# Optimization experiments

Measured on AMD Instinct MI355X. Metric: run time of the kernel, lower is better.

The kernel has to match this reference:

```python
import jax, jax.numpy as jnp
import numpy as np

K = 20
EPS = 1e-5
NEG_SLOPE = 0.2


def knn(x, k):
    # x: [B, C, N] -> idx [B, N, k] of nearest neighbors (negative sq-dist topk)
    inner = -2.0 * jnp.einsum('bcn,bcm->bnm', x, x)
    xx = jnp.sum(x * x, axis=1)  # [B, N]
    d = -xx[:, :, None] - inner - xx[:, None, :]
    return jax.lax.top_k(d, k)[1]


def get_graph_feature(x, k):
    # x: [B, C, N] -> [B, 2C, N, k]
    idx = knn(x, k)
    xt = jnp.transpose(x, (0, 2, 1))            # [B, N, C]
    feat = jax.vmap(lambda a, i: a[i])(xt, idx)  # [B, N, k, C]
    center = xt[:, :, None, :]
    out = jnp.concatenate([feat - center, jnp.broadcast_to(center, feat.shape)], axis=-1)
    return jnp.transpose(out, (0, 3, 1, 2))


def conv_bn_lrelu(x, w, g, b):
    # 1x1 conv + BatchNorm2d (batch stats, training mode) + LeakyReLU(0.2)
    y = jnp.einsum('oc,bcnk->bonk', w, x)
    mu = jnp.mean(y, axis=(0, 2, 3), keepdims=True)
    var = jnp.mean((y - mu) ** 2, axis=(0, 2, 3), keepdims=True)
    y = (y - mu) * jax.lax.rsqrt(var + EPS)
    y = y * g[None, :, None, None] + b[None, :, None, None]
    return jnp.where(y >= 0, y, NEG_SLOPE * y)


def lrelu(y):
    return jnp.where(y >= 0, y, NEG_SLOPE * y)


def setup_inputs() -> dict:
    key = jax.random.key(0)
    ks = jax.random.split(key, 24)
    B, N = 8, 4096
    d = {}
    d['x'] = jax.random.normal(ks[0], (B, 3, N), dtype=jnp.float32)
    def wconv(k_, o, c):
        return jax.random.normal(k_, (o, c), dtype=jnp.float32) * (1.0 / np.sqrt(c))
    d['w1'] = wconv(ks[1], 32, 6)
    d['g1'] = 1.0 + 0.1 * jax.random.normal(ks[2], (32,), dtype=jnp.float32)
    d['b1'] = 0.1 * jax.random.normal(ks[3], (32,), dtype=jnp.float32)
    d['w2'] = wconv(ks[4], 64, 70)
    d['g2'] = 1.0 + 0.1 * jax.random.normal(ks[5], (64,), dtype=jnp.float32)
    d['b2'] = 0.1 * jax.random.normal(ks[6], (64,), dtype=jnp.float32)
    d['wd1'] = wconv(ks[7], 64, 64)
    d['gd1'] = 1.0 + 0.1 * jax.random.normal(ks[8], (64,), dtype=jnp.float32)
    d['bd1'] = 0.1 * jax.random.normal(ks[9], (64,), dtype=jnp.float32)
    d['wd2'] = wconv(ks[10], 64, 128)
    d['gd2'] = 1.0 + 0.1 * jax.random.normal(ks[11], (64,), dtype=jnp.float32)
    d['bd2'] = 0.1 * jax.random.normal(ks[12], (64,), dtype=jnp.float32)
    d['W2d'] = jax.random.normal(ks[13], (128, 128), dtype=jnp.float32) * (1.0 / np.sqrt(128))
    d['b2d'] = 0.1 * jax.random.normal(ks[14], (128,), dtype=jnp.float32)
    d['W3d'] = jax.random.normal(ks[15], (64, 128), dtype=jnp.float32) * (1.0 / np.sqrt(128))
    d['b3d'] = 0.1 * jax.random.normal(ks[16], (64,), dtype=jnp.float32)
    d['W4d'] = jax.random.normal(ks[17], (11, 64), dtype=jnp.float32) * (1.0 / np.sqrt(64))
    d['b4d'] = 0.1 * jax.random.normal(ks[18], (11,), dtype=jnp.float32)
    return d


def reference(x, w1, g1, b1, w2, g2, b2, wd1, gd1, bd1, wd2, gd2, bd2,
              W2d, b2d, W3d, b3d, W4d, b4d):
    x1_gf = get_graph_feature(x, K)                    # [B, 6, N, k]
    x1_max = jnp.max(conv_bn_lrelu(x1_gf, w1, g1, b1), axis=-1)  # [B, 32, N]
    x2_gf = jnp.concatenate([x1_gf, get_graph_feature(x1_max, K)], axis=1)  # [B, 70, N, k]
    x2_max = jnp.max(conv_bn_lrelu(x2_gf, w2, g2, b2), axis=-1)  # [B, 64, N]
    xd1 = jnp.max(conv_bn_lrelu(get_graph_feature(x1_max, K), wd1, gd1, bd1), axis=-1)  # [B, 64, N]
    xd2 = jnp.max(conv_bn_lrelu(get_graph_feature(x2_max, K), wd2, gd2, bd2), axis=-1)  # [B, 64, N]
    h = jnp.concatenate([xd1, xd2], axis=1)            # [B, 128, N]
    h = h.reshape(1, -1, 128)                          # faithful row-major view
    h = jnp.mean(h, axis=1)                            # [1, 128]
    h = lrelu(h @ W2d.T + b2d)
    h = lrelu(h @ W3d.T + b3d)
    return lrelu(h @ W4d.T + b4d)                      # [1, 11]
```

## Files before the change

### kernel.cpp

```cpp
#include <hip/hip_runtime.h>

#define BB 8
#define NN 4096
#define KK 20
constexpr float EPSV = 1e-5f;
constexpr float SLOPE = 0.2f;

typedef __bf16 bfrag __attribute__((ext_vector_type(8)));
typedef float floatx4 __attribute__((ext_vector_type(4)));
typedef unsigned short us4 __attribute__((ext_vector_type(4)));
typedef unsigned short us8 __attribute__((ext_vector_type(8)));

__device__ __forceinline__ float lrelu(float v) { return v >= 0.f ? v : SLOPE * v; }

__device__ __forceinline__ unsigned short bf16rn(float f) {
    unsigned int u = __float_as_uint(f);
    return (unsigned short)((u + 0x7FFFu + ((u >> 16) & 1u)) >> 16);
}
__device__ __forceinline__ float bf16up(unsigned short h) {
    return __uint_as_float(((unsigned int)h) << 16);
}

__device__ __forceinline__ void gl_lds16(const unsigned short* g, unsigned short* l) {
    __builtin_amdgcn_global_load_lds((const __attribute__((address_space(1))) void*)g,
                                     (__attribute__((address_space(3))) void*)l, 16, 0, 0);
}

__global__ void zero_kernel(float* p, int n) {
    int i = blockIdx.x * 256 + threadIdx.x;
    if (i < n) p[i] = 0.f;
}

template<int C>
__global__ void pack_kernel(const float* __restrict__ src, unsigned short* __restrict__ pk) {
    constexpr int SK = 2 * C + 8;
    const int id = blockIdx.x;
    const int b = id & 7;
    const int m0 = (id >> 3) * 64;
    const int tid = threadIdx.x;
    for (int i = tid; i < 64 * (C / 4); i += 256) {
        int m = i & 63;
        int c4 = (i >> 6) * 4;
        us4 hv, lv;
        #pragma unroll
        for (int j = 0; j < 4; j++) {
            float v = src[(b * C + c4 + j) * NN + m0 + m];
            unsigned short h = bf16rn(v);
            hv[j] = h;
            lv[j] = bf16rn(v - bf16up(h));
        }
        *(us4*)(&pk[(size_t)(b * NN + m0 + m) * SK + c4]) = hv;
        *(us4*)(&pk[(size_t)(b * NN + m0 + m) * SK + C + c4]) = lv;
    }
    if (tid < 64) {
        float s = 0.f;
        for (int c = 0; c < C; c++) {
            float v = src[(b * C + c) * NN + m0 + tid];
            s += v * v;
        }
        unsigned int ub = __float_as_uint(0.5f * s);
        us8 z;
        #pragma unroll
        for (int j = 0; j < 8; j++) z[j] = 0;
        z[0] = (unsigned short)(ub & 0xFFFFu);
        z[1] = (unsigned short)(ub >> 16);
        *(us8*)(&pk[(size_t)(b * NN + m0 + tid) * SK + 2 * C]) = z;
    }
}

__global__ void pack3_kernel(const float* __restrict__ src, unsigned short* __restrict__ pk) {
    const int id = blockIdx.x;
    const int b = id & 7;
    const int m = (id >> 3) * 256 + threadIdx.x;
    us8 w0, w1;
    #pragma unroll
    for (int j = 0; j < 8; j++) { w0[j] = 0; w1[j] = 0; }
    unsigned short row[12];
    float s = 0.f;
    #pragma unroll
    for (int c = 0; c < 3; c++) {
        float v = src[(b * 3 + c) * NN + m];
        s += v * v;
        unsigned short h = bf16rn(v);
        unsigned short l = bf16rn(v - bf16up(h));
        row[c] = h; row[3 + c] = l; row[6 + c] = l; row[9 + c] = h;
    }
    #pragma unroll
    for (int j = 0; j < 8; j++) w0[j] = row[j];
    #pragma unroll
    for (int j = 0; j < 4; j++) w1[j] = row[8 + j];
    unsigned short* dst = pk + (size_t)(b * NN + m) * 40;
    us8 z;
    #pragma unroll
    for (int j = 0; j < 8; j++) z[j] = 0;
    unsigned int ub = __float_as_uint(0.5f * s);
    us8 zh = z;
    zh[0] = (unsigned short)(ub & 0xFFFFu);
    zh[1] = (unsigned short)(ub >> 16);
    *(us8*)(dst) = w0;
    *(us8*)(dst + 8) = w1;
    *(us8*)(dst + 16) = z;
    *(us8*)(dst + 24) = z;
    *(us8*)(dst + 32) = zh;
}

template<int C>
__global__ __launch_bounds__(256) void knn_kernel(const float* __restrict__ src,
                                                  const unsigned short* __restrict__ pk,
                                                  int* __restrict__ idx) {
    constexpr int SK = (C == 3) ? 40 : (2 * C + 8);
    constexpr int HNOFF = (C == 3) ? 32 : 2 * C;
    constexpr int UNITS = 8 * SK;
    constexpr int PF = (UNITS + 255) / 256;
    constexpr int KKN = (C == 3) ? 1 : (C / 32);
    __shared__ __attribute__((aligned(16))) unsigned short cpack[2 * 64 * SK];
    __shared__ float pv[64 * 65];
    __shared__ unsigned short pidx[64 * 66];
    __shared__ float tau[64];
    __shared__ int cnt[64];
    __shared__ unsigned short qls[(C == 3) ? 64 * 40 : 2];

    const int bid = blockIdx.x;
    const int b = bid & 7;
    const int q0 = (bid >> 3) * 64;
    const int tid = threadIdx.x;
    const int lane = tid & 63;
    const int wv = tid >> 6;
    const int wr = (wv >> 1) * 32;
    const int wc = (wv & 1) * 32;
    const int fl = lane & 15;
    const int fq = lane >> 4;

    float tv[20]; int ti[20];
    #pragma unroll
    for (int k = 0; k < 20; k++) { tv[k] = -3.4e38f; ti[k] = 0; }

    bfrag qah[KKN][2], qal[KKN][2];
    if (C == 3) {
        for (int i = tid; i < 64 * 20; i += 256) {
            int r = i / 20, k = 12 + i % 20;
            qls[r * 40 + k] = 0;
        }
        if (tid < 64) {
            #pragma unroll
            for (int c = 0; c < 3; c++) {
                float v = src[(b * 3 + c) * NN + q0 + tid];
                unsigned short h = bf16rn(v);
                unsigned short l = bf16rn(v - bf16up(h));
                qls[tid * 40 + c] = h;  qls[tid * 40 + 3 + c] = l;
                qls[tid * 40 + 6 + c] = h;  qls[tid * 40 + 9 + c] = l;
            }
        }
    } else {
        #pragma unroll
        for (int r2 = 0; r2 < 2; r2++) {
            const unsigned short* qr = pk + (size_t)(b * NN + q0 + wr + r2 * 16 + fl) * SK + fq * 8;
            #pragma unroll
            for (int kk = 0; kk < KKN; kk++) {
                qah[kk][r2] = *(const bfrag*)(qr + kk * 32);
                qal[kk][r2] = *(const bfrag*)(qr + C + kk * 32);
            }
        }
    }

    {
        const unsigned short* p0 = pk + (size_t)(b * NN) * SK;
        #pragma unroll
        for (int r = 0; r < PF; r++) {
            int u0 = r * 256 + wv * 64;
            if (u0 < UNITS)
                gl_lds16(p0 + (size_t)(u0 + lane) * 8, cpack + (size_t)u0 * 8);
        }
    }
    if (tid < 64) { tau[tid] = -3.4e38f; cnt[tid] = 0; }
    __syncthreads();

    bfrag qa3[2];
    if (C == 3) {
        #pragma unroll
        for (int r2 = 0; r2 < 2; r2++)
            qa3[r2] = *(const bfrag*)(&qls[(wr + r2 * 16 + fl) * 40 + fq * 8]);
    }

    int buf = 0;
    for (int ch = 0; ch < 64; ch++) {
        unsigned short* cur = cpack + buf * (64 * SK);
        if (ch + 1 < 64) {
            unsigned short* nxt = cpack + (buf ^ 1) * (64 * SK);
            const unsigned short* pn = pk + (size_t)(b * NN + (ch + 1) * 64) * SK;
            #pragma unroll
            for (int r = 0; r < PF; r++) {
                int u0 = r * 256 + wv * 64;
                if (u0 < UNITS)
                    gl_lds16(pn + (size_t)(u0 + lane) * 8, nxt + (size_t)u0 * 8);
            }
        }

        floatx4 acc[2][2];
        #pragma unroll
        for (int r2 = 0; r2 < 2; r2++)
            #pragma unroll
            for (int c2 = 0; c2 < 2; c2++)
                acc[r2][c2] = (floatx4)(0.f);

        if (C == 3) {
            #pragma unroll
            for (int c2 = 0; c2 < 2; c2++) {
                bfrag bm = *(const bfrag*)(&cur[(wc + c2 * 16 + fl) * SK + fq * 8]);
                #pragma unroll
                for (int r2 = 0; r2 < 2; r2++)
                    acc[r2][c2] = __builtin_amdgcn_mfma_f32_16x16x32_bf16(qa3[r2], bm, acc[r2][c2], 0, 0, 0);
            }
        } else {
            #pragma unroll
            for (int kk = 0; kk < KKN; kk++) {
                const int kb = kk * 32 + fq * 8;
                bfrag bh[2], bl[2];
                #pragma unroll
                for (int c2 = 0; c2 < 2; c2++) {
                    bh[c2] = *(const bfrag*)(&cur[(wc + c2 * 16 + fl) * SK + kb]);
                    bl[c2] = *(const bfrag*)(&cur[(wc + c2 * 16 + fl) * SK + C + kb]);
                }
                #pragma unroll
                for (int r2 = 0; r2 < 2; r2++)
                    #pragma unroll
                    for (int c2 = 0; c2 < 2; c2++) {
                        acc[r2][c2] = __builtin_amdgcn_mfma_f32_16x16x32_bf16(qah[kk][r2], bh[c2], acc[r2][c2], 0, 0, 0);
                        acc[r2][c2] = __builtin_amdgcn_mfma_f32_16x16x32_bf16(qah[kk][r2], bl[c2], acc[r2][c2], 0, 0, 0);
                        acc[r2][c2] = __builtin_amdgcn_mfma_f32_16x16x32_bf16(qal[kk][r2], bh[c2], acc[r2][c2], 0, 0, 0);
                        acc[r2][c2] = __builtin_amdgcn_mfma_f32_16x16x32_bf16(qal[kk][r2], bl[c2], acc[r2][c2], 0, 0, 0);
                    }
            }
        }

        {
            const int m0 = ch * 64;
            float hvv[2];
            #pragma unroll
            for (int c2 = 0; c2 < 2; c2++)
                hvv[c2] = *(const float*)(&cur[(wc + c2 * 16 + fl) * SK + HNOFF]);
            #pragma unroll
            for (int r2 = 0; r2 < 2; r2++) {
                const int qb = wr + r2 * 16 + fq * 4;
                float4 t4 = *(const float4*)(&tau[qb]);
                float ta[4] = { t4.x, t4.y, t4.z, t4.w };
                #pragma unroll
                for (int c2 = 0; c2 < 2; c2++) {
                    const float hv = hvv[c2];
                    const int mm = m0 + wc + c2 * 16 + fl;
                    #pragma unroll
                    for (int reg = 0; reg < 4; reg++) {
                        float s = acc[r2][c2][reg] - hv;
                        if (s > ta[reg]) {
                            int q = qb + reg;
                            int p = atomicAdd(&cnt[q], 1);
                            pv[q * 65 + p] = s;
                            pidx[q * 66 + p] = (unsigned short)mm;
                        }
                    }
                }
            }
        }
        __syncthreads();

        if (tid < 64) {
            int n = cnt[tid];
            for (int t = 0; t < n; t++) {
                float v = pv[tid * 65 + t];
                if (v > tv[0]) {
                    tv[0] = v; ti[0] = (int)pidx[tid * 66 + t];
                    #pragma unroll
                    for (int j = 0; j < 19; j++) {
                        if (tv[j] > tv[j + 1]) {
                            float a = tv[j]; tv[j] = tv[j + 1]; tv[j + 1] = a;
                            int bi = ti[j]; ti[j] = ti[j + 1]; ti[j + 1] = bi;
                        }
                    }
                }
            }
            cnt[tid] = 0;
            tau[tid] = tv[0];
        }
        __syncthreads();
        buf ^= 1;
    }

    if (tid < 64) {
        #pragma unroll
        for (int k = 0; k < 20; k++)
            idx[(b * NN + q0 + tid) * KK + k] = ti[k];
    }
}

template<int COUT>
__global__ void precompute_kernel(const float* __restrict__ src, int C,
                                  const float* __restrict__ w, int CIN, int wd_off, int wc_off,
                                  float* __restrict__ G, float* __restrict__ H,
                                  int initG, int initH) {
    constexpr int MY = 256 / COUT;
    extern __shared__ float lds[];
    float* wd = lds;
    float* wc = lds + C * COUT;
    const int id = blockIdx.x;
    const int b = id & 7;
    const int m_base = (id >> 3) * 64;
    const int tid = threadIdx.y * COUT + threadIdx.x;
    for (int i = tid; i < C * COUT; i += 256) {
        int c = i / COUT, o = i % COUT;
        float a  = w[o * CIN + wd_off + c];
        float cc = w[o * CIN + wc_off + c];
        wd[i] = a;
        wc[i] = cc - a;
    }
    __syncthreads();
    const int o = threadIdx.x;
    for (int it = 0; it < COUT / 4; it++) {
        int m = m_base + it * MY + threadIdx.y;
        float g = 0.f, h = 0.f;
        for (int c = 0; c < C; c++) {
            float s = src[(b * C + c) * NN + m];
            g += wd[c * COUT + o] * s;
            h += wc[c * COUT + o] * s;
        }
        int gi = (b * NN + m) * COUT + o;
        if (initG) G[gi] = g; else G[gi] += g;
        if (initH) H[gi] = h; else H[gi] += h;
    }
}

template<int COUT, int GROUPS>
__global__ void conv_stats_kernel(const float* __restrict__ G1, const int* __restrict__ idx1,
                                  const float* __restrict__ G2, const int* __restrict__ idx2,
                                  const float* __restrict__ H, float* __restrict__ stats,
                                  float* __restrict__ MaxY, float* __restrict__ MinY) {
    constexpr int NY = 256 / COUT;
    const int id = blockIdx.x;
    const int b = id & 7;
    const int o = threadIdx.x;
    const int n = (id >> 3) * NY + threadIdx.y;
    const int base = b * NN + n;
    const float h = H[base * COUT + o];
    float s1 = 0.f, s2 = 0.f;
    float gx = -3.4e38f, gn = 3.4e38f;
    #pragma unroll
    for (int k = 0; k < KK; k++) {
        int i1 = idx1[base * KK + k];
        float g = G1[(b * NN + i1) * COUT + o];
        if (GROUPS == 2) {
            int i2 = idx2[base * KK + k];
            g += G2[(b * NN + i2) * COUT + o];
        }
        float y = g + h;
        s1 += y;
        s2 += y * y;
        gx = fmaxf(gx, g);
        gn = fminf(gn, g);
    }
    MaxY[base * COUT + o] = gx + h;
    MinY[base * COUT + o] = gn + h;

    __shared__ float ls[2 * COUT];
    if (threadIdx.y == 0) { ls[o] = 0.f; ls[COUT + o] = 0.f; }
    __syncthreads();
    atomicAdd(&ls[o], s1);
    atomicAdd(&ls[COUT + o], s2);
    __syncthreads();
    if (threadIdx.y == 0) {
        atomicAdd(&stats[o], ls[o]);
        atomicAdd(&stats[64 + o], ls[COUT + o]);
    }
}

__global__ void finalize_kernel(const float* __restrict__ g, const float* __restrict__ bb,
                                float* __restrict__ stats, int cout, float invP) {
    int o = threadIdx.x;
    if (o >= cout) return;
    float mu  = stats[o] * invP;
    float var = stats[64 + o] * invP - mu * mu;
    float sc  = g[o] * rsqrtf(var + EPSV);
    stats[128 + o] = sc;
    stats[192 + o] = bb[o] - mu * sc;
}

__global__ void apply_kernel(const float* __restrict__ MaxY, const float* __restrict__ MinY,
                             const float* __restrict__ stats, float* __restrict__ out, int cout) {
    const int id = blockIdx.x;
    const int b = id & 7;
    int e = (id >> 3) * 256 + threadIdx.x;
    if (e >= cout * NN) return;
    int n = e & (NN - 1);
    int o = e >> 12;
    float sc = stats[128 + o], sh = stats[192 + o];
    int si = (b * NN + n) * cout + o;
    float v = (sc >= 0.f) ? MaxY[si] : MinY[si];
    out[(b * cout + o) * NN + n] = lrelu(sc * v + sh);
}

__global__ void mean_kernel(const float* __restrict__ xd1, const float* __restrict__ xd2,
                            float* __restrict__ hsum) {
    __shared__ float bins[128];
    const int tid = threadIdx.x;
    if (tid < 128) bins[tid] = 0.f;
    __syncthreads();
    const int half = BB * 64 * NN;
    const int stride = gridDim.x * 256;
    for (int e = blockIdx.x * 256 + tid; e < half; e += stride)
        atomicAdd(&bins[e & 127], xd1[e]);
    for (int e = blockIdx.x * 256 + tid; e < half; e += stride)
        atomicAdd(&bins[e & 127], xd2[e]);
    __syncthreads();
    if (tid < 128) atomicAdd(&hsum[tid], bins[tid]);
}

__global__ void head_kernel(const float* __restrict__ hsum,
                            const float* __restrict__ W2d, const float* __restrict__ b2d,
                            const float* __restrict__ W3d, const float* __restrict__ b3d,
                            const float* __restrict__ W4d, const float* __restrict__ b4d,
                            float* __restrict__ out) {
    __shared__ float h[128], t1[128], t2[64];
    const int t = threadIdx.x;
    h[t] = hsum[t] * (1.f / 32768.f);
    __syncthreads();
    float a = b2d[t];
    for (int j = 0; j < 128; j++) a += W2d[t * 128 + j] * h[j];
    t1[t] = lrelu(a);
    __syncthreads();
    if (t < 64) {
        float a2 = b3d[t];
        for (int j = 0; j < 128; j++) a2 += W3d[t * 128 + j] * t1[j];
        t2[t] = lrelu(a2);
    }
    __syncthreads();
    if (t < 11) {
        float a3 = b4d[t];
        for (int j = 0; j < 64; j++) a3 += W4d[t * 64 + j] * t2[j];
        out[t] = lrelu(a3);
    }
}

extern "C" void kernel_launch(void* const* d_in, const int* in_sizes, int n_in,
                              void* d_out, int out_size, void* d_ws, size_t ws_size,
                              hipStream_t stream) {
    const float* x   = (const float*)d_in[0];
    const float* w1  = (const float*)d_in[1];
    const float* g1  = (const float*)d_in[2];
    const float* b1  = (const float*)d_in[3];
    const float* w2  = (const float*)d_in[4];
    const float* g2  = (const float*)d_in[5];
    const float* b2  = (const float*)d_in[6];
    const float* wd1 = (const float*)d_in[7];
    const float* gd1 = (const float*)d_in[8];
    const float* bd1 = (const float*)d_in[9];
    const float* wd2 = (const float*)d_in[10];
    const float* gd2 = (const float*)d_in[11];
    const float* bd2 = (const float*)d_in[12];
    const float* W2d = (const float*)d_in[13];
    const float* b2d = (const float*)d_in[14];
    const float* W3d = (const float*)d_in[15];
    const float* b3d = (const float*)d_in[16];
    const float* W4d = (const float*)d_in[17];
    const float* b4d = (const float*)d_in[18];
    float* out = (float*)d_out;

    char* ws = (char*)d_ws;
    size_t off = 0;
    auto alloc = [&](size_t bytes) { char* p = ws + off; off += (bytes + 255) & ~size_t(255); return p; };
    int*   idx1  = (int*)  alloc(BB * NN * KK * 4);
    int*   idx2  = (int*)  alloc(BB * NN * KK * 4);
    int*   idx3  = (int*)  alloc(BB * NN * KK * 4);
    float* x1m   = (float*)alloc(BB * 32 * NN * 4);
    float* x2m   = (float*)alloc(BB * 64 * NN * 4);
    float* xd1   = (float*)alloc(BB * 64 * NN * 4);
    float* xd2   = (float*)alloc(BB * 64 * NN * 4);
    float* G1    = (float*)alloc((size_t)BB * NN * 64 * 4);
    float* G2    = (float*)alloc((size_t)BB * NN * 64 * 4);
    float* H     = (float*)alloc((size_t)BB * NN * 64 * 4);
    float* MaxY  = (float*)alloc((size_t)BB * NN * 64 * 4);
    float* MinY  = (float*)alloc((size_t)BB * NN * 64 * 4);
    float* stats = (float*)alloc(4 * 256 * 4);
    float* hsum  = (float*)alloc(128 * 4);

    float* st0 = stats;
    float* st1 = stats + 256;
    float* st2 = stats + 512;
    float* st3 = stats + 768;

    unsigned short* pkbuf = (unsigned short*)MaxY;

    const float invP = 1.f / (float)(BB * NN * KK);
    const dim3 knn_grid(NN / 64 * BB);
    const dim3 pre_grid(NN / 64 * BB);

    zero_kernel<<<5, 256, 0, stream>>>(stats, 1024 + 128);

    pack3_kernel<<<NN / 256 * BB, 256, 0, stream>>>(x, pkbuf);
    knn_kernel<3><<<knn_grid, 256, 0, stream>>>(x, pkbuf, idx1);

    precompute_kernel<32><<<pre_grid, dim3(32, 8), 2 * 3 * 32 * 4, stream>>>(
        x, 3, w1, 6, 0, 3, G1, H, 1, 1);
    conv_stats_kernel<32, 1><<<NN / 8 * BB, dim3(32, 8), 0, stream>>>(
        G1, idx1, nullptr, nullptr, H, st0, MaxY, MinY);
    finalize_kernel<<<1, 64, 0, stream>>>(g1, b1, st0, 32, invP);
    apply_kernel<<<32 * NN / 256 * BB, 256, 0, stream>>>(MaxY, MinY, st0, x1m, 32);

    pack_kernel<32><<<pre_grid, 256, 0, stream>>>(x1m, pkbuf);
    knn_kernel<32><<<knn_grid, 256, 0, stream>>>(x1m, pkbuf, idx2);

    precompute_kernel<64><<<pre_grid, dim3(64, 4), 2 * 3 * 64 * 4, stream>>>(
        x, 3, w2, 70, 0, 3, G1, H, 1, 1);
    precompute_kernel<64><<<pre_grid, dim3(64, 4), 2 * 32 * 64 * 4, stream>>>(
        x1m, 32, w2, 70, 6, 38, G2, H, 1, 0);
    conv_stats_kernel<64, 2><<<NN / 4 * BB, dim3(64, 4), 0, stream>>>(
        G1, idx1, G2, idx2, H, st1, MaxY, MinY);
    finalize_kernel<<<1, 64, 0, stream>>>(g2, b2, st1, 64, invP);
    apply_kernel<<<64 * NN / 256 * BB, 256, 0, stream>>>(MaxY, MinY, st1, x2m, 64);

    precompute_kernel<64><<<pre_grid, dim3(64, 4), 2 * 32 * 64 * 4, stream>>>(
        x1m, 32, wd1, 64, 0, 32, G1, H, 1, 1);
    conv_stats_kernel<64, 1><<<NN / 4 * BB, dim3(64, 4), 0, stream>>>(
        G1, idx2, nullptr, nullptr, H, st2, MaxY, MinY);
    finalize_kernel<<<1, 64, 0, stream>>>(gd1, bd1, st2, 64, invP);
    apply_kernel<<<64 * NN / 256 * BB, 256, 0, stream>>>(MaxY, MinY, st2, xd1, 64);

    pack_kernel<64><<<pre_grid, 256, 0, stream>>>(x2m, pkbuf);
    knn_kernel<64><<<knn_grid, 256, 0, stream>>>(x2m, pkbuf, idx3);

    precompute_kernel<64><<<pre_grid, dim3(64, 4), 2 * 64 * 64 * 4, stream>>>(
        x2m, 64, wd2, 128, 0, 64, G1, H, 1, 1);
    conv_stats_kernel<64, 1><<<NN / 4 * BB, dim3(64, 4), 0, stream>>>(
        G1, idx3, nullptr, nullptr, H, st3, MaxY, MinY);
    finalize_kernel<<<1, 64, 0, stream>>>(gd2, bd2, st3, 64, invP);
    apply_kernel<<<64 * NN / 256 * BB, 256, 0, stream>>>(MaxY, MinY, st3, xd2, 64);

    mean_kernel<<<1024, 256, 0, stream>>>(xd1, xd2, hsum);
    head_kernel<<<1, 128, 0, stream>>>(hsum, W2d, b2d, W3d, b3d, W4d, b4d, out);
}
```

Measured before the change: 1.670 ms.

## Select max/min by gamma sign early, fuse finalize into apply, merge precompute

Because rsqrt is positive, the sign of the BN scale equals the sign of gamma. The conv-stats kernel can therefore pick the max or the min per channel immediately and write one value buffer instead of two. The finalize kernel is folded into apply, with each block computing its channel's scale and shift into shared memory. The two precompute passes for the second conv are merged into one kernel that writes G1, G2 and H without read-modify-write. Together these cut memory traffic and the number of launches; the cost is some redundant per-block stats arithmetic.

```diff
diff --git a/kernel.cpp b/kernel.cpp
--- a/kernel.cpp
+++ b/kernel.cpp
@@ -295,8 +295,7 @@
 template<int COUT>
 __global__ void precompute_kernel(const float* __restrict__ src, int C,
                                   const float* __restrict__ w, int CIN, int wd_off, int wc_off,
-                                  float* __restrict__ G, float* __restrict__ H,
-                                  int initG, int initH) {
+                                  float* __restrict__ G, float* __restrict__ H) {
     constexpr int MY = 256 / COUT;
     extern __shared__ float lds[];
     float* wd = lds;
@@ -323,16 +322,58 @@
             h += wc[c * COUT + o] * s;
         }
         int gi = (b * NN + m) * COUT + o;
-        if (initG) G[gi] = g; else G[gi] += g;
-        if (initH) H[gi] = h; else H[gi] += h;
+        G[gi] = g;
+        H[gi] = h;
+    }
+}
+
+__global__ void precompute2_kernel(const float* __restrict__ srcA, const float* __restrict__ srcB,
+                                   const float* __restrict__ w,
+                                   float* __restrict__ GA, float* __restrict__ GB,
+                                   float* __restrict__ H) {
+    constexpr int COUT = 64, CA = 3, CB = 32, CIN = 70;
+    __shared__ float wdA[CA * COUT], wcA[CA * COUT], wdB[CB * COUT], wcB[CB * COUT];
+    const int id = blockIdx.x;
+    const int b = id & 7;
+    const int m_base = (id >> 3) * 64;
+    const int tid = threadIdx.y * COUT + threadIdx.x;
+    for (int i = tid; i < CA * COUT; i += 256) {
+        int c = i / COUT, o = i % COUT;
+        float a = w[o * CIN + 0 + c], cc = w[o * CIN + 3 + c];
+        wdA[i] = a; wcA[i] = cc - a;
+    }
+    for (int i = tid; i < CB * COUT; i += 256) {
+        int c = i / COUT, o = i % COUT;
+        float a = w[o * CIN + 6 + c], cc = w[o * CIN + 38 + c];
+        wdB[i] = a; wcB[i] = cc - a;
+    }
+    __syncthreads();
+    const int o = threadIdx.x;
+    for (int it = 0; it < 16; it++) {
+        int m = m_base + it * 4 + threadIdx.y;
+        float ga = 0.f, gb = 0.f, h = 0.f;
+        for (int c = 0; c < CA; c++) {
+            float s = srcA[(b * CA + c) * NN + m];
+            ga += wdA[c * COUT + o] * s;
+            h  += wcA[c * COUT + o] * s;
+        }
+        for (int c = 0; c < CB; c++) {
+            float s = srcB[(b * CB + c) * NN + m];
+            gb += wdB[c * COUT + o] * s;
+            h  += wcB[c * COUT + o] * s;
+        }
+        int gi = (b * NN + m) * COUT + o;
+        GA[gi] = ga;
+        GB[gi] = gb;
+        H[gi] = h;
     }
 }
 
 template<int COUT, int GROUPS>
 __global__ void conv_stats_kernel(const float* __restrict__ G1, const int* __restrict__ idx1,
                                   const float* __restrict__ G2, const int* __restrict__ idx2,
-                                  const float* __restrict__ H, float* __restrict__ stats,
-                                  float* __restrict__ MaxY, float* __restrict__ MinY) {
+                                  const float* __restrict__ H, const float* __restrict__ gw,
+                                  float* __restrict__ stats, float* __restrict__ V) {
     constexpr int NY = 256 / COUT;
     const int id = blockIdx.x;
     const int b = id & 7;
@@ -356,8 +397,7 @@
         gx = fmaxf(gx, g);
         gn = fminf(gn, g);
     }
-    MaxY[base * COUT + o] = gx + h;
-    MinY[base * COUT + o] = gn + h;
+    V[base * COUT + o] = ((gw[o] >= 0.f) ? gx : gn) + h;
 
     __shared__ float ls[2 * COUT];
     if (threadIdx.y == 0) { ls[o] = 0.f; ls[COUT + o] = 0.f; }
@@ -371,29 +411,25 @@
     }
 }
 
-__global__ void finalize_kernel(const float* __restrict__ g, const float* __restrict__ bb,
-                                float* __restrict__ stats, int cout, float invP) {
-    int o = threadIdx.x;
-    if (o >= cout) return;
-    float mu  = stats[o] * invP;
-    float var = stats[64 + o] * invP - mu * mu;
-    float sc  = g[o] * rsqrtf(var + EPSV);
-    stats[128 + o] = sc;
-    stats[192 + o] = bb[o] - mu * sc;
-}
-
-__global__ void apply_kernel(const float* __restrict__ MaxY, const float* __restrict__ MinY,
-                             const float* __restrict__ stats, float* __restrict__ out, int cout) {
+__global__ void apply_kernel(const float* __restrict__ V, const float* __restrict__ stats,
+                             const float* __restrict__ g, const float* __restrict__ bb,
+                             float* __restrict__ out, int cout, float invP) {
     const int id = blockIdx.x;
     const int b = id & 7;
     int e = (id >> 3) * 256 + threadIdx.x;
-    if (e >= cout * NN) return;
     int n = e & (NN - 1);
     int o = e >> 12;
-    float sc = stats[128 + o], sh = stats[192 + o];
-    int si = (b * NN + n) * cout + o;
-    float v = (sc >= 0.f) ? MaxY[si] : MinY[si];
-    out[(b * cout + o) * NN + n] = lrelu(sc * v + sh);
+    __shared__ float sc_s, sh_s;
+    if (threadIdx.x == 0) {
+        float mu  = stats[o] * invP;
+        float var = stats[64 + o] * invP - mu * mu;
+        float sc  = g[o] * rsqrtf(var + EPSV);
+        sc_s = sc;
+        sh_s = bb[o] - mu * sc;
+    }
+    __syncthreads();
+    float v = V[(b * NN + n) * cout + o];
+    out[(b * cout + o) * NN + n] = lrelu(sc_s * v + sh_s);
 }
 
 __global__ void mean_kernel(const float* __restrict__ xd1, const float* __restrict__ xd2,
@@ -475,17 +511,18 @@
     float* G1    = (float*)alloc((size_t)BB * NN * 64 * 4);
     float* G2    = (float*)alloc((size_t)BB * NN * 64 * 4);
     float* H     = (float*)alloc((size_t)BB * NN * 64 * 4);
-    float* MaxY  = (float*)alloc((size_t)BB * NN * 64 * 4);
-    float* MinY  = (float*)alloc((size_t)BB * NN * 64 * 4);
+    float* Vbuf  = (float*)alloc((size_t)BB * NN * 64 * 4);
+    float* pad   = (float*)alloc((size_t)BB * NN * 64 * 4);
     float* stats = (float*)alloc(4 * 256 * 4);
     float* hsum  = (float*)alloc(128 * 4);
+    (void)pad;
 
     float* st0 = stats;
     float* st1 = stats + 256;
     float* st2 = stats + 512;
     float* st3 = stats + 768;
 
-    unsigned short* pkbuf = (unsigned short*)MaxY;
+    unsigned short* pkbuf = (unsigned short*)Vbuf;
 
     const float invP = 1.f / (float)(BB * NN * KK);
     const dim3 knn_grid(NN / 64 * BB);
@@ -497,40 +534,33 @@
     knn_kernel<3><<<knn_grid, 256, 0, stream>>>(x, pkbuf, idx1);
 
     precompute_kernel<32><<<pre_grid, dim3(32, 8), 2 * 3 * 32 * 4, stream>>>(
-        x, 3, w1, 6, 0, 3, G1, H, 1, 1);
+        x, 3, w1, 6, 0, 3, G1, H);
     conv_stats_kernel<32, 1><<<NN / 8 * BB, dim3(32, 8), 0, stream>>>(
-        G1, idx1, nullptr, nullptr, H, st0, MaxY, MinY);
-    finalize_kernel<<<1, 64, 0, stream>>>(g1, b1, st0, 32, invP);
-    apply_kernel<<<32 * NN / 256 * BB, 256, 0, stream>>>(MaxY, MinY, st0, x1m, 32);
+        G1, idx1, nullptr, nullptr, H, g1, st0, Vbuf);
+    apply_kernel<<<32 * NN / 256 * BB, 256, 0, stream>>>(Vbuf, st0, g1, b1, x1m, 32, invP);
 
     pack_kernel<32><<<pre_grid, 256, 0, stream>>>(x1m, pkbuf);
     knn_kernel<32><<<knn_grid, 256, 0, stream>>>(x1m, pkbuf, idx2);
 
-    precompute_kernel<64><<<pre_grid, dim3(64, 4), 2 * 3 * 64 * 4, stream>>>(
-        x, 3, w2, 70, 0, 3, G1, H, 1, 1);
+    precompute2_kernel<<<pre_grid, dim3(64, 4), 0, stream>>>(x, x1m, w2, G1, G2, H);
+    conv_stats_kernel<64, 2><<<NN / 4 * BB, dim3(64, 4), 0, stream>>>(
+        G1, idx1, G2, idx2, H, g2, st1, Vbuf);
+    apply_kernel<<<64 * NN / 256 * BB, 256, 0, stream>>>(Vbuf, st1, g2, b2, x2m, 64, invP);
+
     precompute_kernel<64><<<pre_grid, dim3(64, 4), 2 * 32 * 64 * 4, stream>>>(
-        x1m, 32, w2, 70, 6, 38, G2, H, 1, 0);
-    conv_stats_kernel<64, 2><<<NN / 4 * BB, dim3(64, 4), 0, stream>>>(
-        G1, idx1, G2, idx2, H, st1, MaxY, MinY);
-    finalize_kernel<<<1, 64, 0, stream>>>(g2, b2, st1, 64, invP);
-    apply_kernel<<<64 * NN / 256 * BB, 256, 0, stream>>>(MaxY, MinY, st1, x2m, 64);
-
-    precompute_kernel<64><<<pre_grid, dim3(64, 4), 2 * 32 * 64 * 4, stream>>>(
-        x1m, 32, wd1, 64, 0, 32, G1, H, 1, 1);
+        x1m, 32, wd1, 64, 0, 32, G2, H);
     conv_stats_kernel<64, 1><<<NN / 4 * BB, dim3(64, 4), 0, stream>>>(
-        G1, idx2, nullptr, nullptr, H, st2, MaxY, MinY);
-    finalize_kernel<<<1, 64, 0, stream>>>(gd1, bd1, st2, 64, invP);
-    apply_kernel<<<64 * NN / 256 * BB, 256, 0, stream>>>(MaxY, MinY, st2, xd1, 64);
+        G2, idx2, nullptr, nullptr, H, gd1, st2, Vbuf);
+    apply_kernel<<<64 * NN / 256 * BB, 256, 0, stream>>>(Vbuf, st2, gd1, bd1, xd1, 64, invP);
 
     pack_kernel<64><<<pre_grid, 256, 0, stream>>>(x2m, pkbuf);
     knn_kernel<64><<<knn_grid, 256, 0, stream>>>(x2m, pkbuf, idx3);
 
     precompute_kernel<64><<<pre_grid, dim3(64, 4), 2 * 64 * 64 * 4, stream>>>(
-        x2m, 64, wd2, 128, 0, 64, G1, H, 1, 1);
+        x2m, 64, wd2, 128, 0, 64, G2, H);
     conv_stats_kernel<64, 1><<<NN / 4 * BB, dim3(64, 4), 0, stream>>>(
-        G1, idx3, nullptr, nullptr, H, st3, MaxY, MinY);
-    finalize_kernel<<<1, 64, 0, stream>>>(gd2, bd2, st3, 64, invP);
-    apply_kernel<<<64 * NN / 256 * BB, 256, 0, stream>>>(MaxY, MinY, st3, xd2, 64);
+        G2, idx3, nullptr, nullptr, H, gd2, st3, Vbuf);
+    apply_kernel<<<64 * NN / 256 * BB, 256, 0, stream>>>(Vbuf, st3, gd2, bd2, xd2, 64, invP);
 
     mean_kernel<<<1024, 256, 0, stream>>>(xd1, xd2, hsum);
     head_kernel<<<1, 128, 0, stream>>>(hsum, W2d, b2d, W3d, b3d, W4d, b4d, out);
```

Result: no change. 1.641 ms (-1.7%).
